# Performance work log

Measured on AMD Instinct MI355X. Metric: run time of the kernel, lower is better.

## Reference

```python
import jax, jax.numpy as jnp
import numpy as np
from jax import lax

# dims: batch, time, in_channels, out_channels, numerator order, denominator order
B, T, I, O, NB, NA = 16, 4096, 32, 32, 3, 2


def setup_inputs() -> dict:
    key = jax.random.key(0)
    k1, k2, k3 = jax.random.split(key, 3)
    u_in = jax.random.normal(k1, (B, T, I), dtype=jnp.float32)
    # parameters initialized as in the module: randn * 0.1
    b_coeff = jax.random.normal(k2, (O, I, NB), dtype=jnp.float32) * 0.1
    a_coeff = jax.random.normal(k3, (O, I, NA), dtype=jnp.float32) * 0.1
    return {"u_in": u_in, "b_coeff": b_coeff, "a_coeff": a_coeff}


def _mimo_filter(u_in, b_coeff, a_coeff):
    """y[b,t,o] = sum_i IIR_{o,i}(u[b,:,i])[t], zero initial conditions.

    Per pair (o,i): y_oi[t] = sum_k b[o,i,k]*u[t-k,i] - sum_j a[o,i,j]*y_oi[t-j].
    """
    dtype = u_in.dtype
    n_b = b_coeff.shape[-1]
    n_a = a_coeff.shape[-1]
    t_len = u_in.shape[1]

    # FIR (numerator) part, vectorized: x[b,t,o,i] = sum_k b[o,i,k] * u[b,t-k,i]
    u_pad = jnp.pad(u_in, ((0, 0), (n_b - 1, 0), (0, 0)))
    # (B, T, I, n_b): lag-k slice of u for each tap k
    u_lags = jnp.stack([u_pad[:, n_b - 1 - k: n_b - 1 - k + t_len, :]
                        for k in range(n_b)], axis=-1)
    x = jnp.einsum('btik,oik->btoi', u_lags, b_coeff)  # (B, T, O, I)

    # IIR (denominator) recursion via scan over time.
    a = a_coeff  # (O, I, n_a)

    def step(y_hist, x_t):
        # y_hist: (B, O, I, n_a) most-recent-first; x_t: (B, O, I)
        y_t = x_t - jnp.einsum('boij,oij->boi', y_hist, a)
        y_hist = jnp.concatenate([y_t[..., None], y_hist[..., :-1]], axis=-1)
        return y_hist, y_t

    x_tfirst = jnp.moveaxis(x, 1, 0)  # (T, B, O, I)
    init = jnp.zeros(x.shape[:1] + x.shape[2:] + (n_a,), dtype=dtype)  # (B,O,I,n_a)
    _, y_pairs = lax.scan(step, init, x_tfirst)  # (T, B, O, I)
    # sum over input channels -> (B, T, O)
    return jnp.moveaxis(y_pairs, 0, 1).sum(axis=-1)


def reference(u_in, b_coeff, a_coeff):
    return _mimo_filter(u_in, b_coeff, a_coeff)
```

## Files before the change

kernel.cpp:

```cpp
#include <hip/hip_runtime.h>

constexpr int B = 16, T = 4096, I = 32, O = 32;
constexpr int C = 32, L = T / C, W = 32;
constexpr int TT = 32, NC = L / TT;

template <int CTRL>
__device__ __forceinline__ float dppmov(float x) {
    return __int_as_float(__builtin_amdgcn_update_dpp(
        0, __float_as_int(x), CTRL, 0xF, 0xF, true));
}
__device__ __forceinline__ float swz16(float x) {
    return __int_as_float(__builtin_amdgcn_ds_swizzle(__float_as_int(x), 0x401F));
}

__global__ __launch_bounds__(256, 8) void mimo_iir_kernel(
    const float* __restrict__ u,
    const float* __restrict__ bcf,
    const float* __restrict__ acf,
    float* __restrict__ out)
{
    const int tid = threadIdx.x;
    const int i  = tid & 31;
    const int g  = tid >> 5;
    const int gg = blockIdx.x * 8 + g;
    const int o  = gg & (O - 1);
    const int bc = gg >> 5;
    const int c  = bc & (C - 1);
    const int b  = bc >> 5;

    const float* bw = bcf + (o * I + i) * 3;
    const float b0 = bw[0], b1 = bw[1], b2 = bw[2];
    const float* aw = acf + (o * I + i) * 2;
    const float na1 = -aw[0], na2 = -aw[1];

    const float* ub = u + ((size_t)b * T) * I + i;
    const int t0 = c * L;

    float y1 = 0.f, y2 = 0.f, u1 = 0.f, u2 = 0.f;
    float y[TT];

    if (c != 0) {
        const int ts = t0 - W;
        u1 = ub[(ts - 1) * I];
        u2 = ub[(ts - 2) * I];
        const float* wp = ub + (size_t)ts * I;
#pragma unroll
        for (int k = 0; k < TT; ++k) y[k] = wp[k * I];
#pragma unroll
        for (int k = 0; k < TT; ++k) {
            const float u0 = y[k];
            const float x  = fmaf(b0, u0, fmaf(b1, u1, b2 * u2));
            const float yy = fmaf(na1, y1, fmaf(na2, y2, x));
            y2 = y1; y1 = yy; u2 = u1; u1 = u0;
        }
    }

    const float* mp = ub + (size_t)t0 * I;
    float* op = out + ((size_t)(b * T + t0) + i) * O + o;

    const bool l4 = i & 16, l3 = i & 8, l2 = i & 4, l1 = i & 2, l0 = i & 1;

    for (int ch = 0; ch < NC; ++ch) {
#pragma unroll
        for (int k = 0; k < TT; ++k) y[k] = mp[k * I];
#pragma unroll
        for (int k = 0; k < TT; ++k) {
            const float u0 = y[k];
            const float x  = fmaf(b0, u0, fmaf(b1, u1, b2 * u2));
            const float yy = fmaf(na1, y1, fmaf(na2, y2, x));
            y2 = y1; y1 = yy; u2 = u1; u1 = u0;
            y[k] = yy;
        }
#pragma unroll
        for (int m = 0; m < 16; ++m) {
            const float keep = l4 ? y[m + 16] : y[m];
            const float give = l4 ? y[m] : y[m + 16];
            y[m] = keep + swz16(give);
        }
#pragma unroll
        for (int m = 0; m < 8; ++m) {
            const float keep = l3 ? y[m + 8] : y[m];
            const float give = l3 ? y[m] : y[m + 8];
            y[m] = keep + dppmov<0x140>(give);
        }
#pragma unroll
        for (int m = 0; m < 4; ++m) {
            const float keep = l2 ? y[m + 4] : y[m];
            const float give = l2 ? y[m] : y[m + 4];
            y[m] = keep + dppmov<0x141>(give);
        }
#pragma unroll
        for (int m = 0; m < 2; ++m) {
            const float keep = l1 ? y[m + 2] : y[m];
            const float give = l1 ? y[m] : y[m + 2];
            y[m] = keep + dppmov<0x4E>(give);
        }
        {
            const float keep = l0 ? y[1] : y[0];
            const float give = l0 ? y[0] : y[1];
            y[0] = keep + dppmov<0xB1>(give);
        }
        *op = y[0];
        op += (size_t)TT * O;
        mp += TT * I;
    }
}

extern "C" void kernel_launch(void* const* d_in, const int* in_sizes, int n_in,
                              void* d_out, int out_size, void* d_ws, size_t ws_size,
                              hipStream_t stream) {
    const float* u   = (const float*)d_in[0];
    const float* bcf = (const float*)d_in[1];
    const float* acf = (const float*)d_in[2];
    float* out = (float*)d_out;

    const int total_threads = B * C * O * 32;
    const int block = 256;
    const int grid = total_threads / block;
    mimo_iir_kernel<<<grid, block, 0, stream>>>(u, bcf, acf, out);
}
```

Measured before the change: 80.26 us.

## Stage input tiles through double-buffered LDS shared across the block's output channels

```diff
diff --git a/kernel.cpp b/kernel.cpp
--- a/kernel.cpp
+++ b/kernel.cpp
@@ -3,6 +3,7 @@
 constexpr int B = 16, T = 4096, I = 32, O = 32;
 constexpr int C = 32, L = T / C, W = 32;
 constexpr int TT = 32, NC = L / TT;
+constexpr int ROWW = 36;
 
 template <int CTRL>
 __device__ __forceinline__ float dppmov(float x) {
@@ -13,12 +14,14 @@
     return __int_as_float(__builtin_amdgcn_ds_swizzle(__float_as_int(x), 0x401F));
 }
 
-__global__ __launch_bounds__(256, 8) void mimo_iir_kernel(
+__global__ __launch_bounds__(256, 4) void mimo_iir_kernel(
     const float* __restrict__ u,
     const float* __restrict__ bcf,
     const float* __restrict__ acf,
     float* __restrict__ out)
 {
+    __shared__ __align__(16) float tile[2][TT][ROWW];
+
     const int tid = threadIdx.x;
     const int i  = tid & 31;
     const int g  = tid >> 5;
@@ -33,36 +36,44 @@
     const float* aw = acf + (o * I + i) * 2;
     const float na1 = -aw[0], na2 = -aw[1];
 
-    const float* ub = u + ((size_t)b * T) * I + i;
+    const float* ubase = u + ((size_t)b * T) * I;
     const int t0 = c * L;
+    const int first = (c == 0) ? 0 : -1;
 
     float y1 = 0.f, y2 = 0.f, u1 = 0.f, u2 = 0.f;
-    float y[TT];
-
     if (c != 0) {
-        const int ts = t0 - W;
-        u1 = ub[(ts - 1) * I];
-        u2 = ub[(ts - 2) * I];
-        const float* wp = ub + (size_t)ts * I;
-#pragma unroll
-        for (int k = 0; k < TT; ++k) y[k] = wp[k * I];
-#pragma unroll
-        for (int k = 0; k < TT; ++k) {
-            const float u0 = y[k];
-            const float x  = fmaf(b0, u0, fmaf(b1, u1, b2 * u2));
-            const float yy = fmaf(na1, y1, fmaf(na2, y2, x));
-            y2 = y1; y1 = yy; u2 = u1; u1 = u0;
-        }
+        u1 = ubase[(size_t)(t0 - W - 1) * I + i];
+        u2 = ubase[(size_t)(t0 - W - 2) * I + i];
     }
 
-    const float* mp = ub + (size_t)t0 * I;
+    const int tw = tid >> 3;
+    const int i4 = (tid & 7) * 4;
+
+    {
+        const int tb = t0 + first * TT;
+        const float4 s = *reinterpret_cast<const float4*>(
+            ubase + (size_t)(tb + tw) * I + i4);
+        *reinterpret_cast<float4*>(&tile[0][tw][i4]) = s;
+    }
+    __syncthreads();
+
+    float y[TT];
+    const bool l4 = i & 16, l3 = i & 8, l2 = i & 4, l1 = i & 2, l0 = i & 1;
     float* op = out + ((size_t)(b * T + t0) + i) * O + o;
 
-    const bool l4 = i & 16, l3 = i & 8, l2 = i & 4, l1 = i & 2, l0 = i & 1;
+    for (int ch = first; ch < NC; ++ch) {
+        const int p = (ch - first) & 1;
+        const bool more = (ch + 1 < NC);
+        float4 stg;
+        if (more) {
+            const int tb = t0 + (ch + 1) * TT;
+            stg = *reinterpret_cast<const float4*>(
+                ubase + (size_t)(tb + tw) * I + i4);
+        }
 
-    for (int ch = 0; ch < NC; ++ch) {
 #pragma unroll
-        for (int k = 0; k < TT; ++k) y[k] = mp[k * I];
+        for (int k = 0; k < TT; ++k) y[k] = tile[p][k][i];
+
 #pragma unroll
         for (int k = 0; k < TT; ++k) {
             const float u0 = y[k];
@@ -71,38 +82,45 @@
             y2 = y1; y1 = yy; u2 = u1; u1 = u0;
             y[k] = yy;
         }
+
+        if (ch >= 0) {
 #pragma unroll
-        for (int m = 0; m < 16; ++m) {
-            const float keep = l4 ? y[m + 16] : y[m];
-            const float give = l4 ? y[m] : y[m + 16];
-            y[m] = keep + swz16(give);
+            for (int m = 0; m < 16; ++m) {
+                const float keep = l4 ? y[m + 16] : y[m];
+                const float give = l4 ? y[m] : y[m + 16];
+                y[m] = keep + swz16(give);
+            }
+#pragma unroll
+            for (int m = 0; m < 8; ++m) {
+                const float keep = l3 ? y[m + 8] : y[m];
+                const float give = l3 ? y[m] : y[m + 8];
+                y[m] = keep + dppmov<0x140>(give);
+            }
+#pragma unroll
+            for (int m = 0; m < 4; ++m) {
+                const float keep = l2 ? y[m + 4] : y[m];
+                const float give = l2 ? y[m] : y[m + 4];
+                y[m] = keep + dppmov<0x141>(give);
+            }
+#pragma unroll
+            for (int m = 0; m < 2; ++m) {
+                const float keep = l1 ? y[m + 2] : y[m];
+                const float give = l1 ? y[m] : y[m + 2];
+                y[m] = keep + dppmov<0x4E>(give);
+            }
+            {
+                const float keep = l0 ? y[1] : y[0];
+                const float give = l0 ? y[0] : y[1];
+                y[0] = keep + dppmov<0xB1>(give);
+            }
+            op[(size_t)ch * TT * O] = y[0];
         }
-#pragma unroll
-        for (int m = 0; m < 8; ++m) {
-            const float keep = l3 ? y[m + 8] : y[m];
-            const float give = l3 ? y[m] : y[m + 8];
-            y[m] = keep + dppmov<0x140>(give);
+
+        if (more) {
+            *reinterpret_cast<float4*>(
+                &tile[p ^ 1][tw][i4]) = stg;
         }
-#pragma unroll
-        for (int m = 0; m < 4; ++m) {
-            const float keep = l2 ? y[m + 4] : y[m];
-            const float give = l2 ? y[m] : y[m + 4];
-            y[m] = keep + dppmov<0x141>(give);
-        }
-#pragma unroll
-        for (int m = 0; m < 2; ++m) {
-            const float keep = l1 ? y[m + 2] : y[m];
-            const float give = l1 ? y[m] : y[m + 2];
-            y[m] = keep + dppmov<0x4E>(give);
-        }
-        {
-            const float keep = l0 ? y[1] : y[0];
-            const float give = l0 ? y[0] : y[1];
-            y[0] = keep + dppmov<0xB1>(give);
-        }
-        *op = y[0];
-        op += (size_t)TT * O;
-        mp += TT * I;
+        __syncthreads();
     }
 }
 
```

Result: faster. 77.31 us (-3.7%).
